# Kernel optimization log

Hardware: AMD Instinct MI355X
Metric: run time of the kernel (lower is better)

Reference implementation:

```python
import jax, jax.numpy as jnp
import numpy as np

B, L, D, H = 2, 1024, 1024, 16
HD = D // H
HIDDEN = 4 * D
EPS = 1e-6
SCALE = HD ** -0.5

# RoPE tables (head_dim is even, so rope_dim == head_dim)
_inv_freq = 1.0 / (10000.0 ** (np.arange(0, HD, 2, dtype=np.float32) / HD))
_freqs = np.arange(L, dtype=np.float32)[:, None] * _inv_freq[None, :]          # [L, HD/2]
COS = jnp.asarray(np.concatenate([np.cos(_freqs), np.cos(_freqs)], -1))        # [L, HD]
SIN = jnp.asarray(np.concatenate([np.sin(_freqs), np.sin(_freqs)], -1))
MASK = jnp.tril(jnp.ones((L, L), dtype=bool))                                   # causal


def _clin(xr, xi, Wr, Wi, br=None, bi=None):
    # complex linear: (a+bi)(c+di), weights stored [out, in] as in torch
    r = xr @ Wr.T - xi @ Wi.T
    i = xr @ Wi.T + xi @ Wr.T
    if br is not None:
        r = r + br
        i = i + bi
    return r, i


def _cln(xr, xi, gr, gi, br, bi):
    mr = xr.mean(-1, keepdims=True)
    mi = xi.mean(-1, keepdims=True)
    cr = xr - mr
    ci = xi - mi
    var = (cr * cr + ci * ci).mean(-1, keepdims=True)
    s = jnp.sqrt(var + EPS)
    nr = cr / s
    ni = ci / s
    return nr * gr - ni * gi + br, nr * gi + ni * gr + bi


def _rot_half(x):
    h = x.shape[-1] // 2
    return jnp.concatenate([-x[..., h:], x[..., :h]], -1)


def _rope(xr, xi):
    # apply same real rotation to real and imag parts (matches torch code)
    return (xr * COS + _rot_half(xr) * SIN, xi * COS + _rot_half(xi) * SIN)


def _split_heads(x):
    return x.reshape(B, L, H, HD).transpose(0, 2, 1, 3)  # [B,H,L,HD]


def _merge_heads(x):
    return x.transpose(0, 2, 1, 3).reshape(B, L, D)


def setup_inputs() -> dict:
    key = jax.random.key(0)
    ks = jax.random.split(key, 20)
    n = lambda k, shape, s=1.0: jax.random.normal(k, shape, dtype=jnp.float32) * s
    s_attn = (2.0 * (D + D)) ** -0.5
    s_fc1 = (2.0 * (D + HIDDEN)) ** -0.5
    s_fc2 = (2.0 * (HIDDEN + D)) ** -0.5
    return {
        'x_real': n(ks[0], (B, L, D)),
        'x_imag': n(ks[1], (B, L, D)),
        'Wq_r': n(ks[2], (D, D), s_attn), 'Wq_i': n(ks[3], (D, D), s_attn),
        'Wk_r': n(ks[4], (D, D), s_attn), 'Wk_i': n(ks[5], (D, D), s_attn),
        'Wv_r': n(ks[6], (D, D), s_attn), 'Wv_i': n(ks[7], (D, D), s_attn),
        'Wo_r': n(ks[8], (D, D), s_attn), 'Wo_i': n(ks[9], (D, D), s_attn),
        'bo_r': jnp.zeros((D,), jnp.float32), 'bo_i': jnp.zeros((D,), jnp.float32),
        'ln1_gr': jnp.ones((D,), jnp.float32), 'ln1_gi': jnp.zeros((D,), jnp.float32),
        'ln1_br': jnp.zeros((D,), jnp.float32), 'ln1_bi': jnp.zeros((D,), jnp.float32),
        'ln2_gr': jnp.ones((D,), jnp.float32), 'ln2_gi': jnp.zeros((D,), jnp.float32),
        'ln2_br': jnp.zeros((D,), jnp.float32), 'ln2_bi': jnp.zeros((D,), jnp.float32),
        'W1_r': n(ks[10], (HIDDEN, D), s_fc1), 'W1_i': n(ks[11], (HIDDEN, D), s_fc1),
        'b1_r': jnp.zeros((HIDDEN,), jnp.float32), 'b1_i': jnp.zeros((HIDDEN,), jnp.float32),
        'W2_r': n(ks[12], (D, HIDDEN), s_fc2), 'W2_i': n(ks[13], (D, HIDDEN), s_fc2),
        'b2_r': jnp.zeros((D,), jnp.float32), 'b2_i': jnp.zeros((D,), jnp.float32),
        'mod_b': n(ks[14], (HIDDEN,), 0.1),
    }


def reference(x_real, x_imag,
              Wq_r, Wq_i, Wk_r, Wk_i, Wv_r, Wv_i, Wo_r, Wo_i, bo_r, bo_i,
              ln1_gr, ln1_gi, ln1_br, ln1_bi, ln2_gr, ln2_gi, ln2_br, ln2_bi,
              W1_r, W1_i, b1_r, b1_i, W2_r, W2_i, b2_r, b2_i, mod_b):
    # --- attention sublayer (pre-LN) ---
    hr, hi = _cln(x_real, x_imag, ln1_gr, ln1_gi, ln1_br, ln1_bi)
    Qr, Qi = _clin(hr, hi, Wq_r, Wq_i)
    Kr, Ki = _clin(hr, hi, Wk_r, Wk_i)
    Vr, Vi = _clin(hr, hi, Wv_r, Wv_i)
    Qr, Qi, Kr, Ki = map(_split_heads, (Qr, Qi, Kr, Ki))
    Vr, Vi = _split_heads(Vr), _split_heads(Vi)
    Qr, Qi = _rope(Qr, Qi)
    Kr, Ki = _rope(Kr, Ki)
    # Hermitian inner product real part: Re(Q K*) = Qr.Kr + Qi.Ki
    scores = (jnp.einsum('bhld,bhmd->bhlm', Qr, Kr)
              + jnp.einsum('bhld,bhmd->bhlm', Qi, Ki)) * SCALE
    scores = jnp.where(MASK, scores, -jnp.inf)
    attn = jax.nn.softmax(scores, axis=-1)
    out_r = _merge_heads(jnp.einsum('bhlm,bhmd->bhld', attn, Vr))
    out_i = _merge_heads(jnp.einsum('bhlm,bhmd->bhld', attn, Vi))
    out_r, out_i = _clin(out_r, out_i, Wo_r, Wo_i, bo_r, bo_i)
    ar = x_real + out_r
    ai = x_imag + out_i
    # --- feed-forward sublayer (pre-LN) ---
    hr, hi = _cln(ar, ai, ln2_gr, ln2_gi, ln2_br, ln2_bi)
    fr, fi = _clin(hr, hi, W1_r, W1_i, b1_r, b1_i)
    # ModReLU: relu(|z| + b) * e^{i angle(z)}
    mag = jnp.sqrt(fr * fr + fi * fi)
    safe = jnp.where(mag > 0, mag, 1.0)
    act = jax.nn.relu(mag + mod_b)
    fr, fi = act * fr / safe, act * fi / safe
    fr, fi = _clin(fr, fi, W2_r, W2_i, b2_r, b2_i)
    return ar + fr, ai + fi
```

## Files before the change

kernel.cpp:

```cpp
#include <hip/hip_runtime.h>

#define Bq 2
#define Lq 1024
#define Dq 1024
#define Hq 16
#define HDq 64
#define HIDq 4096
#define Mq (Bq*Lq)

typedef __bf16 bf16x8 __attribute__((ext_vector_type(8)));
typedef float floatx4 __attribute__((ext_vector_type(4)));
typedef float floatx16 __attribute__((ext_vector_type(16)));

__device__ __forceinline__ unsigned short f2us(float f){
  unsigned u = __builtin_bit_cast(unsigned, f);
  u = u + 0x7fffu + ((u >> 16) & 1u);
  return (unsigned short)(u >> 16);
}

__device__ __forceinline__ void gld16(const unsigned short* g, unsigned short* l){
  __builtin_amdgcn_global_load_lds(
      (const __attribute__((address_space(1))) unsigned int*)g,
      (__attribute__((address_space(3))) unsigned int*)l, 16, 0, 0);
}

__global__ __launch_bounds__(256) void cvt4_kernel(
    const float* __restrict__ s0, const float* __restrict__ s1,
    const float* __restrict__ s2, const float* __restrict__ s3,
    unsigned short* __restrict__ d0, unsigned short* __restrict__ d1,
    unsigned short* __restrict__ d2, unsigned short* __restrict__ d3,
    int n)
{
  const int a = blockIdx.y;
  const float* s = (a==0) ? s0 : (a==1) ? s1 : (a==2) ? s2 : s3;
  unsigned short* d = (a==0) ? d0 : (a==1) ? d1 : (a==2) ? d2 : d3;
  const int i = (blockIdx.x * 256 + threadIdx.x) * 8;
  if (i >= n) return;
  float4 v0 = ((const float4*)(s + i))[0];
  float4 v1 = ((const float4*)(s + i))[1];
  ushort4 o0, o1;
  o0.x=f2us(v0.x); o0.y=f2us(v0.y); o0.z=f2us(v0.z); o0.w=f2us(v0.w);
  o1.x=f2us(v1.x); o1.y=f2us(v1.y); o1.z=f2us(v1.z); o1.w=f2us(v1.w);
  ((ushort4*)(d + i))[0] = o0;
  ((ushort4*)(d + i))[1] = o1;
}

__global__ __launch_bounds__(256) void cln_kernel(
    const float* __restrict__ xr, const float* __restrict__ xi,
    const float* __restrict__ gr, const float* __restrict__ gi,
    const float* __restrict__ br, const float* __restrict__ bi,
    unsigned short* __restrict__ outr, unsigned short* __restrict__ outi)
{
  const int row = blockIdx.x;
  const int t = threadIdx.x;
  const int lane = t & 63, wv = t >> 6;
  __shared__ float sred[8];

  float4 v4r = ((const float4*)(xr + (size_t)row*Dq))[t];
  float4 v4i = ((const float4*)(xi + (size_t)row*Dq))[t];
  float vr[4] = {v4r.x, v4r.y, v4r.z, v4r.w};
  float vi[4] = {v4i.x, v4i.y, v4i.z, v4i.w};
  float sr = vr[0]+vr[1]+vr[2]+vr[3];
  float si = vi[0]+vi[1]+vi[2]+vi[3];
  #pragma unroll
  for (int o=32;o>0;o>>=1){ sr += __shfl_down(sr,o,64); si += __shfl_down(si,o,64); }
  if (lane==0){ sred[wv]=sr; sred[4+wv]=si; }
  __syncthreads();
  float mr = (sred[0]+sred[1]+sred[2]+sred[3]) * (1.0f/Dq);
  float mi = (sred[4]+sred[5]+sred[6]+sred[7]) * (1.0f/Dq);
  float cr[4], ci[4], vs = 0.f;
  #pragma unroll
  for (int j=0;j<4;++j){ cr[j]=vr[j]-mr; ci[j]=vi[j]-mi; vs += cr[j]*cr[j]+ci[j]*ci[j]; }
  #pragma unroll
  for (int o=32;o>0;o>>=1) vs += __shfl_down(vs,o,64);
  __syncthreads();
  if (lane==0) sred[wv]=vs;
  __syncthreads();
  float var = (sred[0]+sred[1]+sred[2]+sred[3]) * (1.0f/Dq);
  float inv = rsqrtf(var + 1e-6f);

  float4 g4r = ((const float4*)gr)[t];
  float4 g4i = ((const float4*)gi)[t];
  float4 b4r = ((const float4*)br)[t];
  float4 b4i = ((const float4*)bi)[t];
  float grf[4] = {g4r.x,g4r.y,g4r.z,g4r.w};
  float gif[4] = {g4i.x,g4i.y,g4i.z,g4i.w};
  float brf[4] = {b4r.x,b4r.y,b4r.z,b4r.w};
  float bif[4] = {b4i.x,b4i.y,b4i.z,b4i.w};
  ushort4 o_r, o_i;
  unsigned short orr[4], oii[4];
  #pragma unroll
  for (int j=0;j<4;++j){
    float nr = cr[j]*inv, ni = ci[j]*inv;
    orr[j] = f2us(nr*grf[j] - ni*gif[j] + brf[j]);
    oii[j] = f2us(nr*gif[j] + ni*grf[j] + bif[j]);
  }
  o_r.x=orr[0]; o_r.y=orr[1]; o_r.z=orr[2]; o_r.w=orr[3];
  o_i.x=oii[0]; o_i.y=oii[1]; o_i.z=oii[2]; o_i.w=oii[3];
  ((ushort4*)(outr + (size_t)row*Dq))[t] = o_r;
  ((ushort4*)(outi + (size_t)row*Dq))[t] = o_i;
}

template<int EPI, bool ROPE, bool SPLIT3>
__global__ __launch_bounds__(256,2) void cgemm_kernel(
    const unsigned short* __restrict__ Ar, const unsigned short* __restrict__ Ai,
    const unsigned short* __restrict__ Wr, const unsigned short* __restrict__ Wi,
    void* __restrict__ Cr0, void* __restrict__ Ci0,
    void* __restrict__ Cr1, void* __restrict__ Ci1,
    void* __restrict__ Cr2, void* __restrict__ Ci2,
    const float* __restrict__ biasR, const float* __restrict__ biasI,
    const float* __restrict__ resR, const float* __restrict__ resI,
    const float* __restrict__ modb,
    int Ndim, int Kdim)
{
  const int t = threadIdx.x;
  const int w = t >> 6, l = t & 63;
  const int l31 = l & 31, lhi = l >> 5;
  const int wm = w >> 1, wn = w & 1;
  const int m0 = blockIdx.x * 64, n0 = blockIdx.y * 128;

  __shared__ __align__(16) unsigned short sAr0[2048], sAi0[2048], sWr0[4096], sWi0[4096];
  __shared__ __align__(16) unsigned short sAr1[2048], sAi1[2048], sWr1[4096], sWi1[4096];

  floatx16 accRR[2], accII[2], accRI[2], accIR[2];
  #pragma unroll
  for (int i=0;i<2;++i){
    #pragma unroll
    for (int r=0;r<16;++r){ accRR[i][r]=0.f; accII[i][r]=0.f; accRI[i][r]=0.f; accIR[i][r]=0.f; }
  }

  const int lnA = t >> 3, cpA = t & 7;
  const int clA = cpA ^ (lnA & 7);
  const int rwA = lnA*2 + (clA >> 2), kcA = clA & 3;
  const unsigned short* pAr = Ar + (size_t)(m0 + rwA)*Kdim + kcA*8;
  const unsigned short* pAi = Ai + (size_t)(m0 + rwA)*Kdim + kcA*8;
  const int dA = t*8;
  const int ln1 = (t+256) >> 3, cp1 = t & 7;
  const int cl1 = cp1 ^ (ln1 & 7);
  const int rw1 = ln1*2 + (cl1 >> 2), kc1 = cl1 & 3;
  const unsigned short* pWr0 = Wr + (size_t)(n0 + rwA)*Kdim + kcA*8;
  const unsigned short* pWi0 = Wi + (size_t)(n0 + rwA)*Kdim + kcA*8;
  const unsigned short* pWr1 = Wr + (size_t)(n0 + rw1)*Kdim + kc1*8;
  const unsigned short* pWi1 = Wi + (size_t)(n0 + rw1)*Kdim + kc1*8;
  const int dW1 = (t+256)*8;

  const int rA = wm*32 + l31;
  const int lnRA = rA >> 1, bA = (rA & 1)*4;
  int aoff[2];
  #pragma unroll
  for (int s=0;s<2;++s) aoff[s] = lnRA*64 + (((bA + s*2 + lhi) ^ (lnRA & 7)) * 8);
  const int rW0 = wn*64 + l31,      lnW0 = rW0 >> 1, bW0 = (rW0 & 1)*4;
  const int rW1 = wn*64 + 32 + l31, lnW1 = rW1 >> 1, bW1 = (rW1 & 1)*4;
  int woff0[2], woff1[2];
  #pragma unroll
  for (int s=0;s<2;++s){
    woff0[s] = lnW0*64 + (((bW0 + s*2 + lhi) ^ (lnW0 & 7)) * 8);
    woff1[s] = lnW1*64 + (((bW1 + s*2 + lhi) ^ (lnW1 & 7)) * 8);
  }

#define STAGEK(SA, SB, SC, SD, KOFF) do{                                   \
    gld16(pAr  + (KOFF), &SA[dA]);                                         \
    gld16(pAi  + (KOFF), &SB[dA]);                                         \
    gld16(pWr0 + (KOFF), &SC[dA]);                                         \
    gld16(pWi0 + (KOFF), &SD[dA]);                                         \
    gld16(pWr1 + (KOFF), &SC[dW1]);                                        \
    gld16(pWi1 + (KOFF), &SD[dW1]);                                        \
  }while(0)

#define COMPUTEK(SA, SB, SC, SD) do{                                       \
    _Pragma("unroll")                                                      \
    for (int s_=0; s_<2; ++s_){                                            \
      bf16x8 fAr  = *(const bf16x8*)&SA[aoff[s_]];                         \
      bf16x8 fAi  = *(const bf16x8*)&SB[aoff[s_]];                         \
      bf16x8 fW0r = *(const bf16x8*)&SC[woff0[s_]];                        \
      bf16x8 fW0i = *(const bf16x8*)&SD[woff0[s_]];                        \
      bf16x8 fW1r = *(const bf16x8*)&SC[woff1[s_]];                        \
      bf16x8 fW1i = *(const bf16x8*)&SD[woff1[s_]];                        \
      accRR[0] = __builtin_amdgcn_mfma_f32_32x32x16_bf16(fAr, fW0r, accRR[0], 0,0,0); \
      accII[0] = __builtin_amdgcn_mfma_f32_32x32x16_bf16(fAi, fW0i, accII[0], 0,0,0); \
      accRI[0] = __builtin_amdgcn_mfma_f32_32x32x16_bf16(fAr, fW0i, accRI[0], 0,0,0); \
      accIR[0] = __builtin_amdgcn_mfma_f32_32x32x16_bf16(fAi, fW0r, accIR[0], 0,0,0); \
      accRR[1] = __builtin_amdgcn_mfma_f32_32x32x16_bf16(fAr, fW1r, accRR[1], 0,0,0); \
      accII[1] = __builtin_amdgcn_mfma_f32_32x32x16_bf16(fAi, fW1i, accII[1], 0,0,0); \
      accRI[1] = __builtin_amdgcn_mfma_f32_32x32x16_bf16(fAr, fW1i, accRI[1], 0,0,0); \
      accIR[1] = __builtin_amdgcn_mfma_f32_32x32x16_bf16(fAi, fW1r, accIR[1], 0,0,0); \
    } }while(0)

  const int nk = Kdim >> 5;
  STAGEK(sAr0, sAi0, sWr0, sWi0, 0);
  __syncthreads();
  for (int kk=0; kk<nk; kk+=2){
    STAGEK(sAr1, sAi1, sWr1, sWi1, (size_t)(kk+1)*32);
    COMPUTEK(sAr0, sAi0, sWr0, sWi0);
    __syncthreads();
    if (kk+2 < nk) STAGEK(sAr0, sAi0, sWr0, sWi0, (size_t)(kk+2)*32);
    COMPUTEK(sAr1, sAi1, sWr1, sWi1);
    __syncthreads();
  }
#undef STAGEK
#undef COMPUTEK

  float cr[2][16], ci[2][16];
  #pragma unroll
  for (int nf=0; nf<2; ++nf)
    #pragma unroll
    for (int r=0;r<16;++r){
      cr[nf][r] = accRR[nf][r] - accII[nf][r];
      ci[nf][r] = accRI[nf][r] + accIR[nf][r];
    }

  const bool doRope = ROPE && (!SPLIT3 || (n0 < 2048));
  if (doRope){
    const float invf = powf(10000.0f, -(float)l31 * (1.0f/32.0f));
    #pragma unroll
    for (int r=0;r<16;++r){
      const int gm = m0 + wm*32 + (r&3) + 8*(r>>2) + 4*lhi;
      float s, c;
      sincosf((float)(gm & (Lq-1)) * invf, &s, &c);
      float xr_ = cr[0][r], yr_ = cr[1][r];
      cr[0][r] = xr_*c - yr_*s;  cr[1][r] = yr_*c + xr_*s;
      float xi_ = ci[0][r], yi_ = ci[1][r];
      ci[0][r] = xi_*c - yi_*s;  ci[1][r] = yi_*c + xi_*s;
    }
  }

  unsigned short *oR16 = nullptr, *oI16 = nullptr;
  float *oR32 = nullptr, *oI32 = nullptr;
  int ncol0, Nst;
  if (SPLIT3){
    const int aid = n0 >> 10;
    void* vr = (aid==0) ? Cr0 : ((aid==1) ? Cr1 : Cr2);
    void* vi = (aid==0) ? Ci0 : ((aid==1) ? Ci1 : Ci2);
    oR16 = (unsigned short*)vr; oI16 = (unsigned short*)vi;
    ncol0 = n0 & 1023; Nst = 1024;
  } else {
    oR16 = (unsigned short*)Cr0; oI16 = (unsigned short*)Ci0;
    oR32 = (float*)Cr0;          oI32 = (float*)Ci0;
    ncol0 = n0; Nst = Ndim;
  }

  #pragma unroll
  for (int nf=0; nf<2; ++nf){
    const int gn = n0 + wn*64 + nf*32 + l31;
    const int cn = ncol0 + wn*64 + nf*32 + l31;
    float bR = 0.f, bI = 0.f, mb = 0.f;
    if (EPI >= 1){ bR = biasR[gn]; bI = biasI[gn]; }
    if (EPI == 2){ mb = modb[gn]; }
    #pragma unroll
    for (int r=0;r<16;++r){
      const int gm = m0 + wm*32 + (r&3) + 8*(r>>2) + 4*lhi;
      const size_t idx = (size_t)gm*Nst + cn;
      float vr_ = cr[nf][r] + bR, vi_ = ci[nf][r] + bI;
      if (EPI == 1 || EPI == 3){ vr_ += resR[idx]; vi_ += resI[idx]; }
      if (EPI == 2){
        float mag = sqrtf(vr_*vr_ + vi_*vi_);
        float safe = (mag > 0.f) ? mag : 1.0f;
        float act = fmaxf(mag + mb, 0.f);
        float sc = act / safe;
        vr_ *= sc; vi_ *= sc;
      }
      if (EPI == 0 || EPI == 2){
        oR16[idx] = f2us(vr_);
        oI16[idx] = f2us(vi_);
      } else {
        oR32[idx] = vr_;
        oI32[idx] = vi_;
      }
    }
  }
}

__global__ __launch_bounds__(256) void vtrans_kernel(
    const unsigned short* __restrict__ Vr, const unsigned short* __restrict__ Vi,
    unsigned short* __restrict__ VTr, unsigned short* __restrict__ VTi)
{
  const int lt = blockIdx.x;
  const int bh = blockIdx.y;
  const int h = bh & (Hq-1), b = bh >> 4;
  const int t = threadIdx.x;
  __shared__ unsigned short sTr[64*65], sTi[64*65];

  const int row = t >> 2;
  const int dc  = (t & 3) * 16;
  const size_t g = ((size_t)(b*Lq) + lt*64 + row)*Dq + h*HDq + dc;
  uint4 a0 = *(const uint4*)(Vr + g);
  uint4 a1 = *(const uint4*)(Vr + g + 8);
  uint4 b0 = *(const uint4*)(Vi + g);
  uint4 b1 = *(const uint4*)(Vi + g + 8);
  const unsigned short* pa0 = (const unsigned short*)&a0;
  const unsigned short* pa1 = (const unsigned short*)&a1;
  const unsigned short* pb0 = (const unsigned short*)&b0;
  const unsigned short* pb1 = (const unsigned short*)&b1;
  #pragma unroll
  for (int e=0;e<8;++e){
    sTr[(dc+e)*65 + row]   = pa0[e];
    sTr[(dc+8+e)*65 + row] = pa1[e];
    sTi[(dc+e)*65 + row]   = pb0[e];
    sTi[(dc+8+e)*65 + row] = pb1[e];
  }
  __syncthreads();
  const int d  = t >> 2;
  const int lcx = (t & 3) * 16;
  unsigned short bufr[16], bufi[16];
  #pragma unroll
  for (int e=0;e<16;++e){
    bufr[e] = sTr[d*65 + lcx + e];
    bufi[e] = sTi[d*65 + lcx + e];
  }
  const size_t og = ((size_t)bh*HDq + d)*Lq + lt*64 + lcx;
  *(uint4*)(VTr + og)     = *(const uint4*)&bufr[0];
  *(uint4*)(VTr + og + 8) = *(const uint4*)&bufr[8];
  *(uint4*)(VTi + og)     = *(const uint4*)&bufi[0];
  *(uint4*)(VTi + og + 8) = *(const uint4*)&bufi[8];
}

__device__ __forceinline__ int swz(int v){ return v ^ ((v >> 4) & 7); }

__global__ __launch_bounds__(256,2) void fattn_kernel(
    const unsigned short* __restrict__ Qr, const unsigned short* __restrict__ Qi,
    const unsigned short* __restrict__ Kr, const unsigned short* __restrict__ Ki,
    const unsigned short* __restrict__ VTr, const unsigned short* __restrict__ VTi,
    unsigned short* __restrict__ Or, unsigned short* __restrict__ Oi)
{
  const int qt = (int)(gridDim.x - 1 - blockIdx.x);
  const int bh = blockIdx.y;
  const int h = bh & (Hq-1), b = bh >> 4;
  const int t = threadIdx.x;
  const int w = t >> 6, lane = t & 63;
  const int quad = lane >> 4, l15 = lane & 15;

  __shared__ __align__(16) unsigned short sKr[4096], sKi[4096], sVr[4096], sVi[4096];
  __shared__ __align__(16) unsigned short sP[64*72];

  const size_t qbase = ((size_t)(b*Lq) + qt*64 + w*16 + l15)*Dq + h*HDq;
  bf16x8 qr_lo = *(const bf16x8*)(Qr + qbase + quad*8);
  bf16x8 qr_hi = *(const bf16x8*)(Qr + qbase + 32 + quad*8);
  bf16x8 qi_lo = *(const bf16x8*)(Qi + qbase + quad*8);
  bf16x8 qi_hi = *(const bf16x8*)(Qi + qbase + 32 + quad*8);

  const floatx4 fzero = {0.f,0.f,0.f,0.f};
  floatx4 aOr[4], aOi[4];
  #pragma unroll
  for (int i=0;i<4;++i){ aOr[i]=fzero; aOi[i]=fzero; }
  float m_run[4] = {-1e30f,-1e30f,-1e30f,-1e30f};
  float l_run[4] = {0.f,0.f,0.f,0.f};

  const int srow = t >> 2;
  const int sns  = srow >> 4;
  const int sl15 = srow & 15;
  const int q8   = (t & 3) * 2;
  const int dstA = sns*1024 + swz(q8*16 + sl15)*8;
  const int dstB = sns*1024 + swz((q8+1)*16 + sl15)*8;

  const int rd0 = swz(quad*16 + l15)*8;
  const int rd1 = swz((4+quad)*16 + l15)*8;

  for (int kt = 0; kt <= qt; ++kt){
    const size_t kg = ((size_t)(b*Lq) + kt*64 + srow)*Dq + h*HDq + q8*8;
    uint4 ka = *(const uint4*)(Kr + kg);
    uint4 kb = *(const uint4*)(Kr + kg + 8);
    uint4 kc = *(const uint4*)(Ki + kg);
    uint4 kd = *(const uint4*)(Ki + kg + 8);
    const size_t vg = ((size_t)bh*HDq + srow)*Lq + kt*64 + q8*8;
    uint4 va = *(const uint4*)(VTr + vg);
    uint4 vb = *(const uint4*)(VTr + vg + 8);
    uint4 vc = *(const uint4*)(VTi + vg);
    uint4 vd = *(const uint4*)(VTi + vg + 8);
    __syncthreads();
    *(uint4*)&sKr[dstA] = ka;  *(uint4*)&sKr[dstB] = kb;
    *(uint4*)&sKi[dstA] = kc;  *(uint4*)&sKi[dstB] = kd;
    *(uint4*)&sVr[dstA] = va;  *(uint4*)&sVr[dstB] = vb;
    *(uint4*)&sVi[dstA] = vc;  *(uint4*)&sVi[dstB] = vd;
    __syncthreads();

    floatx4 sc[4];
    #pragma unroll
    for (int ns=0; ns<4; ++ns){
      floatx4 x = fzero;
      x = __builtin_amdgcn_mfma_f32_16x16x32_bf16(qr_lo, *(const bf16x8*)&sKr[ns*1024 + rd0], x, 0,0,0);
      x = __builtin_amdgcn_mfma_f32_16x16x32_bf16(qr_hi, *(const bf16x8*)&sKr[ns*1024 + rd1], x, 0,0,0);
      x = __builtin_amdgcn_mfma_f32_16x16x32_bf16(qi_lo, *(const bf16x8*)&sKi[ns*1024 + rd0], x, 0,0,0);
      x = __builtin_amdgcn_mfma_f32_16x16x32_bf16(qi_hi, *(const bf16x8*)&sKi[ns*1024 + rd1], x, 0,0,0);
      sc[ns] = x;
    }

    const bool diag = (kt == qt);
    float rmax[4] = {-1e30f,-1e30f,-1e30f,-1e30f};
    #pragma unroll
    for (int ns=0; ns<4; ++ns){
      #pragma unroll
      for (int r=0; r<4; ++r){
        float s = sc[ns][r] * 0.125f;
        if (diag && (ns*16 + l15 > w*16 + quad*4 + r)) s = -1e30f;
        sc[ns][r] = s;
        rmax[r] = fmaxf(rmax[r], s);
      }
    }
    #pragma unroll
    for (int off=1; off<16; off<<=1){
      #pragma unroll
      for (int r=0; r<4; ++r) rmax[r] = fmaxf(rmax[r], __shfl_xor(rmax[r], off, 64));
    }

    float alpha[4], rsum[4];
    #pragma unroll
    for (int r=0; r<4; ++r){
      float mn = fmaxf(m_run[r], rmax[r]);
      alpha[r] = __expf(m_run[r] - mn);
      m_run[r] = mn;
      rsum[r] = 0.f;
    }
    #pragma unroll
    for (int ns=0; ns<4; ++ns){
      #pragma unroll
      for (int r=0; r<4; ++r){
        float p = __expf(sc[ns][r] - m_run[r]);
        rsum[r] += p;
        sP[(w*16 + quad*4 + r)*72 + ns*16 + l15] = f2us(p);
      }
    }
    #pragma unroll
    for (int off=1; off<16; off<<=1){
      #pragma unroll
      for (int r=0; r<4; ++r) rsum[r] += __shfl_xor(rsum[r], off, 64);
    }
    #pragma unroll
    for (int r=0; r<4; ++r) l_run[r] = l_run[r]*alpha[r] + rsum[r];
    #pragma unroll
    for (int ds=0; ds<4; ++ds)
      #pragma unroll
      for (int r=0; r<4; ++r){ aOr[ds][r] *= alpha[r]; aOi[ds][r] *= alpha[r]; }

    #pragma unroll
    for (int step=0; step<2; ++step){
      bf16x8 pf = *(const bf16x8*)&sP[(w*16 + l15)*72 + step*32 + quad*8];
      const int ro = (step==0) ? rd0 : rd1;
      #pragma unroll
      for (int ds=0; ds<4; ++ds){
        aOr[ds] = __builtin_amdgcn_mfma_f32_16x16x32_bf16(pf, *(const bf16x8*)&sVr[ds*1024 + ro], aOr[ds], 0,0,0);
        aOi[ds] = __builtin_amdgcn_mfma_f32_16x16x32_bf16(pf, *(const bf16x8*)&sVi[ds*1024 + ro], aOi[ds], 0,0,0);
      }
    }
  }

  #pragma unroll
  for (int r=0; r<4; ++r){
    const float il = 1.0f / l_run[r];
    const size_t ob = ((size_t)(b*Lq) + qt*64 + w*16 + quad*4 + r)*Dq + h*HDq;
    #pragma unroll
    for (int ds=0; ds<4; ++ds){
      Or[ob + ds*16 + l15] = f2us(aOr[ds][r] * il);
      Oi[ob + ds*16 + l15] = f2us(aOi[ds][r] * il);
    }
  }
}

extern "C" void kernel_launch(void* const* d_in, const int* in_sizes, int n_in,
                              void* d_out, int out_size, void* d_ws, size_t ws_size,
                              hipStream_t stream)
{
  const float* x_r    = (const float*)d_in[0];
  const float* x_i    = (const float*)d_in[1];
  const float* Wq_r   = (const float*)d_in[2];
  const float* Wq_i   = (const float*)d_in[3];
  const float* Wk_r   = (const float*)d_in[4];
  const float* Wk_i   = (const float*)d_in[5];
  const float* Wv_r   = (const float*)d_in[6];
  const float* Wv_i   = (const float*)d_in[7];
  const float* Wo_r   = (const float*)d_in[8];
  const float* Wo_i   = (const float*)d_in[9];
  const float* bo_r   = (const float*)d_in[10];
  const float* bo_i   = (const float*)d_in[11];
  const float* ln1_gr = (const float*)d_in[12];
  const float* ln1_gi = (const float*)d_in[13];
  const float* ln1_br = (const float*)d_in[14];
  const float* ln1_bi = (const float*)d_in[15];
  const float* ln2_gr = (const float*)d_in[16];
  const float* ln2_gi = (const float*)d_in[17];
  const float* ln2_br = (const float*)d_in[18];
  const float* ln2_bi = (const float*)d_in[19];
  const float* W1_r   = (const float*)d_in[20];
  const float* W1_i   = (const float*)d_in[21];
  const float* b1_r   = (const float*)d_in[22];
  const float* b1_i   = (const float*)d_in[23];
  const float* W2_r   = (const float*)d_in[24];
  const float* W2_i   = (const float*)d_in[25];
  const float* b2_r   = (const float*)d_in[26];
  const float* b2_i   = (const float*)d_in[27];
  const float* mod_b  = (const float*)d_in[28];

  char* wsb = (char*)d_ws;
  const size_t MB = 1024*1024;
  unsigned short* bQKV_r = (unsigned short*)(wsb + 0*MB);
  unsigned short* bQKV_i = (unsigned short*)(wsb + 6*MB);
  unsigned short* bWo_r = (unsigned short*)(wsb + 12*MB);
  unsigned short* bWo_i = (unsigned short*)(wsb + 14*MB);
  unsigned short* bW1_r = (unsigned short*)(wsb + 16*MB);
  unsigned short* bW1_i = (unsigned short*)(wsb + 24*MB);
  unsigned short* bW2_r = (unsigned short*)(wsb + 32*MB);
  unsigned short* bW2_i = (unsigned short*)(wsb + 40*MB);
  unsigned short* hr  = (unsigned short*)(wsb + 48*MB);
  unsigned short* hi_ = (unsigned short*)(wsb + 52*MB);
  unsigned short* Qr  = (unsigned short*)(wsb + 56*MB);
  unsigned short* Qi  = (unsigned short*)(wsb + 60*MB);
  unsigned short* Kr  = (unsigned short*)(wsb + 64*MB);
  unsigned short* Ki  = (unsigned short*)(wsb + 68*MB);
  unsigned short* Vr  = (unsigned short*)(wsb + 72*MB);
  unsigned short* Vi  = (unsigned short*)(wsb + 76*MB);
  unsigned short* VTr = (unsigned short*)(wsb + 80*MB);
  unsigned short* VTi = (unsigned short*)(wsb + 84*MB);
  unsigned short* Or  = hr;
  unsigned short* Oi  = hi_;
  unsigned short* h2r = Qr;
  unsigned short* h2i = Qi;
  unsigned short* fr  = (unsigned short*)(wsb + 64*MB);
  unsigned short* fi  = (unsigned short*)(wsb + 80*MB);

  float* outR = (float*)d_out;
  float* outI = outR + (size_t)Mq*Dq;

  const dim3 blk(256);

  const int nDD = Dq*Dq;
  const int nDH = Dq*HIDq;
  cvt4_kernel<<<dim3(nDD/2048, 4), blk, 0, stream>>>(Wq_r, Wk_r, Wv_r, Wo_r,
      bQKV_r, bQKV_r + (size_t)nDD, bQKV_r + (size_t)2*nDD, bWo_r, nDD);
  cvt4_kernel<<<dim3(nDD/2048, 4), blk, 0, stream>>>(Wq_i, Wk_i, Wv_i, Wo_i,
      bQKV_i, bQKV_i + (size_t)nDD, bQKV_i + (size_t)2*nDD, bWo_i, nDD);
  cvt4_kernel<<<dim3(nDH/2048, 4), blk, 0, stream>>>(W1_r, W1_i, W2_r, W2_i,
      bW1_r, bW1_i, bW2_r, bW2_i, nDH);

  cln_kernel<<<Mq, blk, 0, stream>>>(x_r, x_i, ln1_gr, ln1_gi, ln1_br, ln1_bi, hr, hi_);
  cgemm_kernel<0,true,true><<<dim3(Mq/64, 3072/128), blk, 0, stream>>>(
      hr, hi_, bQKV_r, bQKV_i,
      Qr, Qi, Kr, Ki, Vr, Vi,
      nullptr, nullptr, nullptr, nullptr, nullptr, 3072, Dq);
  vtrans_kernel<<<dim3(16, 32), blk, 0, stream>>>(Vr, Vi, VTr, VTi);
  fattn_kernel<<<dim3(16, 32), blk, 0, stream>>>(Qr, Qi, Kr, Ki, VTr, VTi, Or, Oi);
  cgemm_kernel<1,false,false><<<dim3(Mq/64, Dq/128), blk, 0, stream>>>(
      Or, Oi, bWo_r, bWo_i, outR, outI, nullptr, nullptr, nullptr, nullptr,
      bo_r, bo_i, x_r, x_i, nullptr, Dq, Dq);
  cln_kernel<<<Mq, blk, 0, stream>>>(outR, outI, ln2_gr, ln2_gi, ln2_br, ln2_bi, h2r, h2i);
  cgemm_kernel<2,false,false><<<dim3(Mq/64, HIDq/128), blk, 0, stream>>>(
      h2r, h2i, bW1_r, bW1_i, fr, fi, nullptr, nullptr, nullptr, nullptr,
      b1_r, b1_i, nullptr, nullptr, mod_b, HIDq, Dq);
  cgemm_kernel<3,false,false><<<dim3(Mq/64, Dq/128), blk, 0, stream>>>(
      fr, fi, bW2_r, bW2_i, outR, outI, nullptr, nullptr, nullptr, nullptr,
      b2_r, b2_i, outR, outI, nullptr, Dq, HIDq);
}
```

Measured before the change: 530.5 us.

## Split-K the output-projection and FC2 complex GEMMs with a separate reduction kernel

Adds a SPLITK template parameter so the Wo GEMM (split 2) and the FC2 GEMM (split 4) run with more blocks along a z-dimension. Each block writes fp32 partial sums to workspace, and a new reduction kernel adds the partials plus bias and residual. Both GEMMs have only 256 blocks (32x8), which may underfill the GPU, especially FC2 with its long K=4096 loop. In exchange it adds extra fp32 partial writes and reads plus one more launch per GEMM. The split path only runs when the workspace is at least 160MB.

```diff
diff --git a/kernel.cpp b/kernel.cpp
--- a/kernel.cpp
+++ b/kernel.cpp
@@ -101,7 +101,7 @@
   ((ushort4*)(outi + (size_t)row*Dq))[t] = o_i;
 }
 
-template<int EPI, bool ROPE, bool SPLIT3>
+template<int EPI, bool ROPE, bool SPLIT3, int SPLITK>
 __global__ __launch_bounds__(256,2) void cgemm_kernel(
     const unsigned short* __restrict__ Ar, const unsigned short* __restrict__ Ai,
     const unsigned short* __restrict__ Wr, const unsigned short* __restrict__ Wi,
@@ -118,6 +118,8 @@
   const int l31 = l & 31, lhi = l >> 5;
   const int wm = w >> 1, wn = w & 1;
   const int m0 = blockIdx.x * 64, n0 = blockIdx.y * 128;
+  const int kbase = (SPLITK > 1) ? (int)blockIdx.z * (Kdim / SPLITK) : 0;
+  const int Klen = Kdim / SPLITK;
 
   __shared__ __align__(16) unsigned short sAr0[2048], sAi0[2048], sWr0[4096], sWi0[4096];
   __shared__ __align__(16) unsigned short sAr1[2048], sAi1[2048], sWr1[4096], sWi1[4096];
@@ -132,16 +134,16 @@
   const int lnA = t >> 3, cpA = t & 7;
   const int clA = cpA ^ (lnA & 7);
   const int rwA = lnA*2 + (clA >> 2), kcA = clA & 3;
-  const unsigned short* pAr = Ar + (size_t)(m0 + rwA)*Kdim + kcA*8;
-  const unsigned short* pAi = Ai + (size_t)(m0 + rwA)*Kdim + kcA*8;
+  const unsigned short* pAr = Ar + (size_t)(m0 + rwA)*Kdim + kcA*8 + kbase;
+  const unsigned short* pAi = Ai + (size_t)(m0 + rwA)*Kdim + kcA*8 + kbase;
   const int dA = t*8;
   const int ln1 = (t+256) >> 3, cp1 = t & 7;
   const int cl1 = cp1 ^ (ln1 & 7);
   const int rw1 = ln1*2 + (cl1 >> 2), kc1 = cl1 & 3;
-  const unsigned short* pWr0 = Wr + (size_t)(n0 + rwA)*Kdim + kcA*8;
-  const unsigned short* pWi0 = Wi + (size_t)(n0 + rwA)*Kdim + kcA*8;
-  const unsigned short* pWr1 = Wr + (size_t)(n0 + rw1)*Kdim + kc1*8;
-  const unsigned short* pWi1 = Wi + (size_t)(n0 + rw1)*Kdim + kc1*8;
+  const unsigned short* pWr0 = Wr + (size_t)(n0 + rwA)*Kdim + kcA*8 + kbase;
+  const unsigned short* pWi0 = Wi + (size_t)(n0 + rwA)*Kdim + kcA*8 + kbase;
+  const unsigned short* pWr1 = Wr + (size_t)(n0 + rw1)*Kdim + kc1*8 + kbase;
+  const unsigned short* pWi1 = Wi + (size_t)(n0 + rw1)*Kdim + kc1*8 + kbase;
   const int dW1 = (t+256)*8;
 
   const int rA = wm*32 + l31;
@@ -186,7 +188,7 @@
       accIR[1] = __builtin_amdgcn_mfma_f32_32x32x16_bf16(fAi, fW1r, accIR[1], 0,0,0); \
     } }while(0)
 
-  const int nk = Kdim >> 5;
+  const int nk = Klen >> 5;
   STAGEK(sAr0, sAi0, sWr0, sWi0, 0);
   __syncthreads();
   for (int kk=0; kk<nk; kk+=2){
@@ -238,13 +240,18 @@
     oR32 = (float*)Cr0;          oI32 = (float*)Ci0;
     ncol0 = n0; Nst = Ndim;
   }
+  if (EPI == 4){
+    const size_t pstride = (size_t)Mq * Ndim;
+    oR32 = (float*)Cr0 + (size_t)blockIdx.z * pstride;
+    oI32 = (float*)Ci0 + (size_t)blockIdx.z * pstride;
+  }
 
   #pragma unroll
   for (int nf=0; nf<2; ++nf){
     const int gn = n0 + wn*64 + nf*32 + l31;
     const int cn = ncol0 + wn*64 + nf*32 + l31;
     float bR = 0.f, bI = 0.f, mb = 0.f;
-    if (EPI >= 1){ bR = biasR[gn]; bI = biasI[gn]; }
+    if (EPI >= 1 && EPI <= 3){ bR = biasR[gn]; bI = biasI[gn]; }
     if (EPI == 2){ mb = modb[gn]; }
     #pragma unroll
     for (int r=0;r<16;++r){
@@ -268,6 +275,35 @@
       }
     }
   }
+}
+
+template<int NS>
+__global__ __launch_bounds__(256) void redk_kernel(
+    const float* __restrict__ pR, const float* __restrict__ pI,
+    const float* __restrict__ bR, const float* __restrict__ bI,
+    const float* __restrict__ rR, const float* __restrict__ rI,
+    float* __restrict__ oR, float* __restrict__ oI)
+{
+  const size_t MN = (size_t)Mq * Dq;
+  const size_t i = ((size_t)blockIdx.x * 256 + threadIdx.x) * 4;
+  const int col = (int)(i & (Dq - 1));
+  float4 br = *(const float4*)(bR + col);
+  float4 bi = *(const float4*)(bI + col);
+  float4 xr = *(const float4*)(rR + i);
+  float4 xi = *(const float4*)(rI + i);
+  float ar0 = br.x + xr.x, ar1 = br.y + xr.y, ar2 = br.z + xr.z, ar3 = br.w + xr.w;
+  float ai0 = bi.x + xi.x, ai1 = bi.y + xi.y, ai2 = bi.z + xi.z, ai3 = bi.w + xi.w;
+  #pragma unroll
+  for (int s=0; s<NS; ++s){
+    float4 qr = *(const float4*)(pR + s*MN + i);
+    float4 qi = *(const float4*)(pI + s*MN + i);
+    ar0 += qr.x; ar1 += qr.y; ar2 += qr.z; ar3 += qr.w;
+    ai0 += qi.x; ai1 += qi.y; ai2 += qi.z; ai3 += qi.w;
+  }
+  float4 orv = {ar0, ar1, ar2, ar3};
+  float4 oiv = {ai0, ai1, ai2, ai3};
+  *(float4*)(oR + i) = orv;
+  *(float4*)(oI + i) = oiv;
 }
 
 __global__ __launch_bounds__(256) void vtrans_kernel(
@@ -515,6 +551,9 @@
   unsigned short* h2i = Qi;
   unsigned short* fr  = (unsigned short*)(wsb + 64*MB);
   unsigned short* fi  = (unsigned short*)(wsb + 80*MB);
+  float* pR = (float*)(wsb + 96*MB);
+  float* pI = (float*)(wsb + 128*MB);
+  const bool can_split = (ws_size >= (size_t)160*MB);
 
   float* outR = (float*)d_out;
   float* outI = outR + (size_t)Mq*Dq;
@@ -531,20 +570,36 @@
       bW1_r, bW1_i, bW2_r, bW2_i, nDH);
 
   cln_kernel<<<Mq, blk, 0, stream>>>(x_r, x_i, ln1_gr, ln1_gi, ln1_br, ln1_bi, hr, hi_);
-  cgemm_kernel<0,true,true><<<dim3(Mq/64, 3072/128), blk, 0, stream>>>(
+  cgemm_kernel<0,true,true,1><<<dim3(Mq/64, 3072/128), blk, 0, stream>>>(
       hr, hi_, bQKV_r, bQKV_i,
       Qr, Qi, Kr, Ki, Vr, Vi,
       nullptr, nullptr, nullptr, nullptr, nullptr, 3072, Dq);
   vtrans_kernel<<<dim3(16, 32), blk, 0, stream>>>(Vr, Vi, VTr, VTi);
   fattn_kernel<<<dim3(16, 32), blk, 0, stream>>>(Qr, Qi, Kr, Ki, VTr, VTi, Or, Oi);
-  cgemm_kernel<1,false,false><<<dim3(Mq/64, Dq/128), blk, 0, stream>>>(
-      Or, Oi, bWo_r, bWo_i, outR, outI, nullptr, nullptr, nullptr, nullptr,
-      bo_r, bo_i, x_r, x_i, nullptr, Dq, Dq);
+  if (can_split){
+    cgemm_kernel<4,false,false,2><<<dim3(Mq/64, Dq/128, 2), blk, 0, stream>>>(
+        Or, Oi, bWo_r, bWo_i, pR, pI, nullptr, nullptr, nullptr, nullptr,
+        nullptr, nullptr, nullptr, nullptr, nullptr, Dq, Dq);
+    redk_kernel<2><<<dim3((Mq*Dq)/1024), blk, 0, stream>>>(
+        pR, pI, bo_r, bo_i, x_r, x_i, outR, outI);
+  } else {
+    cgemm_kernel<1,false,false,1><<<dim3(Mq/64, Dq/128), blk, 0, stream>>>(
+        Or, Oi, bWo_r, bWo_i, outR, outI, nullptr, nullptr, nullptr, nullptr,
+        bo_r, bo_i, x_r, x_i, nullptr, Dq, Dq);
+  }
   cln_kernel<<<Mq, blk, 0, stream>>>(outR, outI, ln2_gr, ln2_gi, ln2_br, ln2_bi, h2r, h2i);
-  cgemm_kernel<2,false,false><<<dim3(Mq/64, HIDq/128), blk, 0, stream>>>(
+  cgemm_kernel<2,false,false,1><<<dim3(Mq/64, HIDq/128), blk, 0, stream>>>(
       h2r, h2i, bW1_r, bW1_i, fr, fi, nullptr, nullptr, nullptr, nullptr,
       b1_r, b1_i, nullptr, nullptr, mod_b, HIDq, Dq);
-  cgemm_kernel<3,false,false><<<dim3(Mq/64, Dq/128), blk, 0, stream>>>(
-      fr, fi, bW2_r, bW2_i, outR, outI, nullptr, nullptr, nullptr, nullptr,
-      b2_r, b2_i, outR, outI, nullptr, Dq, HIDq);
-}
+  if (can_split){
+    cgemm_kernel<4,false,false,4><<<dim3(Mq/64, Dq/128, 4), blk, 0, stream>>>(
+        fr, fi, bW2_r, bW2_i, pR, pI, nullptr, nullptr, nullptr, nullptr,
+        nullptr, nullptr, nullptr, nullptr, nullptr, Dq, HIDq);
+    redk_kernel<4><<<dim3((Mq*Dq)/1024), blk, 0, stream>>>(
+        pR, pI, b2_r, b2_i, outR, outI, outR, outI);
+  } else {
+    cgemm_kernel<3,false,false,1><<<dim3(Mq/64, Dq/128), blk, 0, stream>>>(
+        fr, fi, bW2_r, bW2_i, outR, outI, nullptr, nullptr, nullptr, nullptr,
+        b2_r, b2_i, outR, outI, nullptr, Dq, HIDq);
+  }
+}
```

Result: no change. 523.1 us (-1.4%).
